# Kernel tuning notes

Measured on AMD Instinct MI355X. Metric: run time of the kernel, lower is better.

## Reference

```python
import jax, jax.numpy as jnp
import numpy as np

B, S, D, H = 4, 2048, 768, 12
DK = D // H


def setup_inputs() -> dict:
    key = jax.random.key(0)
    ks = jax.random.split(key, 12)
    s = 1.0 / np.sqrt(D)
    return {
        "query": jax.random.normal(ks[0], (B, S, D), jnp.float32),
        "key_": jax.random.normal(ks[1], (B, S, D), jnp.float32),
        "value": jax.random.normal(ks[2], (B, S, D), jnp.float32),
        "mask": jax.random.randint(ks[3], (B, S), 0, 2, jnp.int32),
        # nn.Linear weights are (out_features, in_features); y = x @ W.T + b
        "Wq": jax.random.normal(ks[4], (D, D), jnp.float32) * s,
        "bq": jnp.zeros((D,), jnp.float32),
        "Wk": jax.random.normal(ks[5], (D, D), jnp.float32) * s,
        "bk": jnp.zeros((D,), jnp.float32),
        "Wv": jax.random.normal(ks[6], (D, D), jnp.float32) * s,
        "bv": jnp.zeros((D,), jnp.float32),
        "Wo": jax.random.normal(ks[7], (D, D), jnp.float32) * s,
        "bo": jnp.zeros((D,), jnp.float32),
    }


def reference(query, key_, value, mask, Wq, bq, Wk, bk, Wv, bv, Wo, bo):
    b = query.shape[0]
    # QKV projections, split heads: (B, S, D) -> (B, H, S, DK)
    def proj(x, W, bia):
        y = x @ W.T + bia
        return y.reshape(b, -1, H, DK).transpose(0, 2, 1, 3)

    q = proj(query, Wq, bq)
    k = proj(key_, Wk, bk)
    v = proj(value, Wv, bv)

    # Scaled dot-product attention with full [B, H, S, S] score matrix
    scores = jnp.einsum("bhqd,bhkd->bhqk", q, k) / jnp.sqrt(jnp.float32(DK))
    # mask: (B, S) broadcast over heads and query positions; masked_fill(mask==0, -1e9)
    scores = jnp.where(mask[:, None, None, :] == 0, jnp.float32(-1e9), scores)
    attn = jax.nn.softmax(scores, axis=-1)
    x = jnp.einsum("bhqk,bhkd->bhqd", attn, v)  # (B, H, S, DK)

    # merge heads and output projection
    x = x.transpose(0, 2, 1, 3).reshape(b, -1, H * DK)
    return x @ Wo.T + bo
```

## Files before the change

### kernel.cpp

```cpp
#include <hip/hip_runtime.h>
#include <math.h>

#define B_  4
#define S_  2048
#define D_  768
#define H_  12
#define DK_ 64
#define M_  (B_ * S_)
#define NBH_ (B_ * H_)

typedef float f32x4 __attribute__((ext_vector_type(4)));
typedef float f32x16 __attribute__((ext_vector_type(16)));
typedef __bf16 bf16x8 __attribute__((ext_vector_type(8)));
typedef unsigned u32x4v __attribute__((ext_vector_type(4)));

static __device__ __forceinline__ unsigned short f2bf(float f) {
    unsigned u = __builtin_bit_cast(unsigned, f);
    u += 0x7fffu + ((u >> 16) & 1u);
    return (unsigned short)(u >> 16);
}

static __device__ __forceinline__ unsigned cvt_pk_bf16(float lo, float hi) {
    unsigned r;
    asm("v_cvt_pk_bf16_f32 %0, %1, %2" : "=v"(r) : "v"(lo), "v"(hi));
    return r;
}

static __device__ __forceinline__ void proj_body(
    const float* __restrict__ X, const float* __restrict__ W,
    const float* __restrict__ bias, void* __restrict__ outp, const int mode,
    const float oscale)
{
    __shared__ __align__(16) unsigned short As[128 * 32];
    __shared__ __align__(16) unsigned short Bs[128 * 32];

    const int t  = threadIdx.x;
    const int l  = t & 63;
    const int w  = t >> 6;
    const int lr = l & 15;
    const int lg = l >> 4;
    const int wm = w >> 1;
    const int wn = w & 1;
    const int m0 = blockIdx.x * 128;
    const int n0 = blockIdx.y * 128;

    f32x4 acc[4][4];
#pragma unroll
    for (int mi = 0; mi < 4; mi++)
#pragma unroll
        for (int ni = 0; ni < 4; ni++) acc[mi][ni] = (f32x4){0.f, 0.f, 0.f, 0.f};

    const int fsw = (lr >> 1) & 3;

    for (int k0 = 0; k0 < D_; k0 += 32) {
#pragma unroll
        for (int i = 0; i < 2; i++) {
            int v    = t + i * 256;
            int row  = v >> 2;
            int so   = v & 3;
            const float* xp = X + (size_t)(m0 + row) * D_ + k0 + so * 8;
            float4 x0 = *(const float4*)(xp);
            float4 x1 = *(const float4*)(xp + 4);
            ushort4 pa, pb;
            pa.x = f2bf(x0.x); pa.y = f2bf(x0.y); pa.z = f2bf(x0.z); pa.w = f2bf(x0.w);
            pb.x = f2bf(x1.x); pb.y = f2bf(x1.y); pb.z = f2bf(x1.z); pb.w = f2bf(x1.w);
            int off = row * 32 + ((so ^ ((row >> 1) & 3)) << 3);
            *(ushort4*)&As[off]     = pa;
            *(ushort4*)&As[off + 4] = pb;

            const float* wp = W + (size_t)(n0 + row) * D_ + k0 + so * 8;
            float4 w0 = *(const float4*)(wp);
            float4 w1 = *(const float4*)(wp + 4);
            pa.x = f2bf(w0.x); pa.y = f2bf(w0.y); pa.z = f2bf(w0.z); pa.w = f2bf(w0.w);
            pb.x = f2bf(w1.x); pb.y = f2bf(w1.y); pb.z = f2bf(w1.z); pb.w = f2bf(w1.w);
            *(ushort4*)&Bs[off]     = pa;
            *(ushort4*)&Bs[off + 4] = pb;
        }
        __syncthreads();

        bf16x8 af[4], bfr[4];
#pragma unroll
        for (int mi = 0; mi < 4; mi++) {
            int row = wm * 64 + mi * 16 + lr;
            af[mi] = *(const bf16x8*)&As[row * 32 + ((lg ^ fsw) << 3)];
        }
#pragma unroll
        for (int ni = 0; ni < 4; ni++) {
            int row = wn * 64 + ni * 16 + lr;
            bfr[ni] = *(const bf16x8*)&Bs[row * 32 + ((lg ^ fsw) << 3)];
        }
#pragma unroll
        for (int mi = 0; mi < 4; mi++)
#pragma unroll
            for (int ni = 0; ni < 4; ni++)
                acc[mi][ni] = __builtin_amdgcn_mfma_f32_16x16x32_bf16(
                    af[mi], bfr[ni], acc[mi][ni], 0, 0, 0);
        __syncthreads();
    }

    const int mrow0 = m0 + wm * 64;
    const int ncol0 = n0 + wn * 64;
    if (mode == 1) {
        float* out = (float*)outp;
#pragma unroll
        for (int mi = 0; mi < 4; mi++)
#pragma unroll
            for (int ni = 0; ni < 4; ni++) {
                int n = ncol0 + ni * 16 + lr;
                float bv = bias[n];
#pragma unroll
                for (int j = 0; j < 4; j++) {
                    int m = mrow0 + mi * 16 + 4 * lg + j;
                    out[(size_t)m * D_ + n] = acc[mi][ni][j] + bv;
                }
            }
    } else if (mode == 0) {
        unsigned short* out = (unsigned short*)outp;
#pragma unroll
        for (int mi = 0; mi < 4; mi++)
#pragma unroll
            for (int ni = 0; ni < 4; ni++) {
                int n = ncol0 + ni * 16 + lr;
                int h = n >> 6, dk = n & 63;
                float bv = bias[n];
#pragma unroll
                for (int j = 0; j < 4; j++) {
                    int m = mrow0 + mi * 16 + 4 * lg + j;
                    int b = m >> 11, s = m & (S_ - 1);
                    out[((size_t)(b * H_ + h) * S_ + s) * DK_ + dk] =
                        f2bf((acc[mi][ni][j] + bv) * oscale);
                }
            }
    } else {
        unsigned short* out = (unsigned short*)outp;
#pragma unroll
        for (int mi = 0; mi < 4; mi++)
#pragma unroll
            for (int ni = 0; ni < 4; ni++) {
                int n = ncol0 + ni * 16 + lr;
                int h = n >> 6, dk = n & 63;
                float bv = bias[n];
                int m = mrow0 + mi * 16 + 4 * lg;
                int b = m >> 11, s = m & (S_ - 1);
                ushort4 o;
                o.x = f2bf(acc[mi][ni][0] + bv);
                o.y = f2bf(acc[mi][ni][1] + bv);
                o.z = f2bf(acc[mi][ni][2] + bv);
                o.w = f2bf(acc[mi][ni][3] + bv);
                *(ushort4*)&out[((size_t)(b * H_ + h) * DK_ + dk) * S_ + s] = o;
            }
    }
}

__global__ __launch_bounds__(256) void proj_qkv(
    const float* __restrict__ Xq, const float* __restrict__ Xk,
    const float* __restrict__ Xv,
    const float* __restrict__ Wq, const float* __restrict__ bq,
    const float* __restrict__ Wk, const float* __restrict__ bk,
    const float* __restrict__ Wv, const float* __restrict__ bv,
    unsigned short* __restrict__ Qb, unsigned short* __restrict__ Kb,
    unsigned short* __restrict__ VT)
{
    const int z = blockIdx.z;
    const float* X    = (z == 0) ? Xq : (z == 1) ? Xk : Xv;
    const float* W    = (z == 0) ? Wq : (z == 1) ? Wk : Wv;
    const float* bias = (z == 0) ? bq : (z == 1) ? bk : bv;
    void* out         = (z == 0) ? (void*)Qb : (z == 1) ? (void*)Kb : (void*)VT;
    const int mode    = (z == 2) ? 2 : 0;
    const float osc   = (z == 0) ? 0.125f : 1.0f;
    proj_body(X, W, bias, out, mode, osc);
}

__global__ __launch_bounds__(256) void proj_mfma(
    const float* __restrict__ X, const float* __restrict__ W,
    const float* __restrict__ bias, void* __restrict__ outp, const int mode,
    const float oscale)
{
    proj_body(X, W, bias, outp, mode, oscale);
}

__global__ __launch_bounds__(256) void attn_mfma(
    const unsigned short* __restrict__ Qb, const unsigned short* __restrict__ Kb,
    const unsigned short* __restrict__ VTb, const int* __restrict__ mask,
    float* __restrict__ O)
{
    __shared__ __align__(16) unsigned short Ks[2][64 * 64];
    __shared__ __align__(16) unsigned short Vs[2][64 * 64];

    const int tid = threadIdx.x;
    const int w  = tid >> 6;
    const int l  = tid & 63;
    const int q  = l & 31;
    const int hl = l >> 5;

    const int bh = blockIdx.x % NBH_;
    const int qt = blockIdx.x / NBH_;
    const int b  = bh / H_;
    const int hh = bh - b * H_;
    const int q0 = qt * 128 + w * 32;

    const unsigned short* qp = Qb + ((size_t)bh * S_ + q0 + q) * DK_;
    bf16x8 qf[4];
#pragma unroll
    for (int c = 0; c < 4; c++)
        qf[c] = *(const bf16x8*)(qp + c * 16 + hl * 8);

    const unsigned qext_sel = (hl == 0) ? 0x00003F80u : 0u;
    const unsigned bias_sel = (hl == 0) ? 0x0000C480u : 0u;
    u32x4v qe; qe.x = qext_sel; qe.y = 0u; qe.z = 0u; qe.w = 0u;
    const bf16x8 qf_ext = __builtin_bit_cast(bf16x8, qe);
    u32x4v on; on.x = on.y = on.z = on.w = 0x3F803F80u;
    const bf16x8 vOnes = __builtin_bit_cast(bf16x8, on);

    f32x16 acc0, acc1, accl;
#pragma unroll
    for (int i = 0; i < 16; i++) { acc0[i] = 0.f; acc1[i] = 0.f; accl[i] = 0.f; }

    const unsigned short* kbase = Kb + (size_t)bh * S_ * DK_;
    const unsigned short* vbase = VTb + (size_t)bh * DK_ * S_;
    const int* mbase = mask + b * S_;

    const int row0 = tid >> 3,         slot0 = tid & 7;
    const int row1 = (tid + 256) >> 3, slot1 = (tid + 256) & 7;
    const int ld0 = row0 * 64 + ((slot0 * 8) ^ ((row0 & 7) << 3));
    const int ld1 = row1 * 64 + ((slot1 * 8) ^ ((row1 & 7) << 3));
    const unsigned short* kg0 = kbase + row0 * DK_ + slot0 * 8;
    const unsigned short* kg1 = kbase + row1 * DK_ + slot1 * 8;
    const unsigned short* vg0 = vbase + (size_t)row0 * S_ + slot0 * 8;
    const unsigned short* vg1 = vbase + (size_t)row1 * S_ + slot1 * 8;

    {
        int4 kr0 = *(const int4*)(kg0);
        int4 kr1 = *(const int4*)(kg1);
        int4 vr0 = *(const int4*)(vg0);
        int4 vr1 = *(const int4*)(vg1);
        *(int4*)&Ks[0][ld0] = kr0;
        *(int4*)&Ks[0][ld1] = kr1;
        *(int4*)&Vs[0][ld0] = vr0;
        *(int4*)&Vs[0][ld1] = vr1;
    }
    __syncthreads();

    const int fsw = (q & 7) << 3;

    for (int tt = 0; tt < 32; tt++) {
        const int j0  = tt * 64;
        const int cur = tt & 1;
        const bool more = (tt < 31);

        int4 kr0, kr1, vr0, vr1;
        if (more) {
            kr0 = *(const int4*)(kg0 + (size_t)(j0 + 64) * DK_);
            kr1 = *(const int4*)(kg1 + (size_t)(j0 + 64) * DK_);
            vr0 = *(const int4*)(vg0 + (j0 + 64));
            vr1 = *(const int4*)(vg1 + (j0 + 64));
        }

        int mv0 = mbase[j0 + q];
        int mv1 = mbase[j0 + 32 + q];
        u32x4v bw0; bw0.x = (mv0 == 0) ? bias_sel : 0u; bw0.y = 0u; bw0.z = 0u; bw0.w = 0u;
        u32x4v bw1; bw1.x = (mv1 == 0) ? bias_sel : 0u; bw1.y = 0u; bw1.z = 0u; bw1.w = 0u;
        bf16x8 kExt0 = __builtin_bit_cast(bf16x8, bw0);
        bf16x8 kExt1 = __builtin_bit_cast(bf16x8, bw1);

        bf16x8 kA[2][4];
#pragma unroll
        for (int kf = 0; kf < 2; kf++)
#pragma unroll
            for (int c = 0; c < 4; c++)
                kA[kf][c] = *(const bf16x8*)&Ks[cur][(32 * kf + q) * 64 +
                                ((c * 16 + hl * 8) ^ fsw)];

        f32x16 s0, s1;
#pragma unroll
        for (int i = 0; i < 16; i++) { s0[i] = 0.f; s1[i] = 0.f; }
        __builtin_amdgcn_s_setprio(1);
#pragma unroll
        for (int c = 0; c < 4; c++) {
            s0 = __builtin_amdgcn_mfma_f32_32x32x16_bf16(kA[0][c], qf[c], s0, 0, 0, 0);
            s1 = __builtin_amdgcn_mfma_f32_32x32x16_bf16(kA[1][c], qf[c], s1, 0, 0, 0);
        }
        s0 = __builtin_amdgcn_mfma_f32_32x32x16_bf16(kExt0, qf_ext, s0, 0, 0, 0);
        s1 = __builtin_amdgcn_mfma_f32_32x32x16_bf16(kExt1, qf_ext, s1, 0, 0, 0);
        __builtin_amdgcn_s_setprio(0);

        bf16x8 vA[2][4];
#pragma unroll
        for (int db = 0; db < 2; db++)
#pragma unroll
            for (int c = 0; c < 4; c++)
                vA[db][c] = *(const bf16x8*)&Vs[cur][(32 * db + q) * 64 +
                                ((c * 16 + hl * 8) ^ fsw)];

        float pv[2][16];
#pragma unroll
        for (int r = 0; r < 16; r++) pv[0][r] = __expf(s0[r]);
#pragma unroll
        for (int r = 0; r < 16; r++) pv[1][r] = __expf(s1[r]);

        bf16x8 pb[4];
#pragma unroll
        for (int cp = 0; cp < 4; cp++) {
            const int kfi = cp >> 1;
            const int e0  = 8 * (cp & 1);
            unsigned lo0 = cvt_pk_bf16(pv[kfi][e0 + 0], pv[kfi][e0 + 1]);
            unsigned hi0 = cvt_pk_bf16(pv[kfi][e0 + 2], pv[kfi][e0 + 3]);
            unsigned lo1 = cvt_pk_bf16(pv[kfi][e0 + 4], pv[kfi][e0 + 5]);
            unsigned hi1 = cvt_pk_bf16(pv[kfi][e0 + 6], pv[kfi][e0 + 7]);
            asm("v_permlane32_swap_b32 %0, %1" : "+v"(lo0), "+v"(lo1));
            asm("v_permlane32_swap_b32 %0, %1" : "+v"(hi0), "+v"(hi1));
            u32x4v pw;
            pw.x = lo0; pw.y = hi0; pw.z = lo1; pw.w = hi1;
            pb[cp] = __builtin_bit_cast(bf16x8, pw);
        }

        __builtin_amdgcn_s_setprio(1);
#pragma unroll
        for (int cp = 0; cp < 4; cp++) {
            acc0 = __builtin_amdgcn_mfma_f32_32x32x16_bf16(vA[0][cp], pb[cp], acc0, 0, 0, 0);
            acc1 = __builtin_amdgcn_mfma_f32_32x32x16_bf16(vA[1][cp], pb[cp], acc1, 0, 0, 0);
            accl = __builtin_amdgcn_mfma_f32_32x32x16_bf16(vOnes,    pb[cp], accl, 0, 0, 0);
        }
        __builtin_amdgcn_s_setprio(0);

        if (more) {
            *(int4*)&Ks[cur ^ 1][ld0] = kr0;
            *(int4*)&Ks[cur ^ 1][ld1] = kr1;
            *(int4*)&Vs[cur ^ 1][ld0] = vr0;
            *(int4*)&Vs[cur ^ 1][ld1] = vr1;
        }
        __syncthreads();
    }

    float inv = 1.f / accl[0];
    float* ob = O + ((size_t)b * S_ + q0 + q) * D_ + hh * DK_;
#pragma unroll
    for (int b2 = 0; b2 < 4; b2++) {
        float4 o;
        o.x = acc0[4 * b2 + 0] * inv;
        o.y = acc0[4 * b2 + 1] * inv;
        o.z = acc0[4 * b2 + 2] * inv;
        o.w = acc0[4 * b2 + 3] * inv;
        *(float4*)(ob + 8 * b2 + 4 * hl) = o;
    }
#pragma unroll
    for (int b2 = 0; b2 < 4; b2++) {
        float4 o;
        o.x = acc1[4 * b2 + 0] * inv;
        o.y = acc1[4 * b2 + 1] * inv;
        o.z = acc1[4 * b2 + 2] * inv;
        o.w = acc1[4 * b2 + 3] * inv;
        *(float4*)(ob + 32 + 8 * b2 + 4 * hl) = o;
    }
}

extern "C" void kernel_launch(void* const* d_in, const int* in_sizes, int n_in,
                              void* d_out, int out_size, void* d_ws, size_t ws_size,
                              hipStream_t stream) {
    (void)in_sizes; (void)n_in; (void)out_size; (void)ws_size;

    const float* query = (const float*)d_in[0];
    const float* key_  = (const float*)d_in[1];
    const float* value = (const float*)d_in[2];
    const int*   mask  = (const int*)d_in[3];
    const float* Wq = (const float*)d_in[4];  const float* bq = (const float*)d_in[5];
    const float* Wk = (const float*)d_in[6];  const float* bk = (const float*)d_in[7];
    const float* Wv = (const float*)d_in[8];  const float* bv = (const float*)d_in[9];
    const float* Wo = (const float*)d_in[10]; const float* bo = (const float*)d_in[11];
    float* out = (float*)d_out;

    unsigned short* Qb = (unsigned short*)d_ws;
    unsigned short* Kb = Qb + (size_t)M_ * D_;
    unsigned short* VT = Kb + (size_t)M_ * D_;
    float*          Xb = (float*)(VT + (size_t)M_ * D_);

    dim3 gqkv(M_ / 128, D_ / 128, 3);
    proj_qkv<<<gqkv, 256, 0, stream>>>(query, key_, value,
                                       Wq, bq, Wk, bk, Wv, bv, Qb, Kb, VT);

    attn_mfma<<<dim3((S_ / 128) * NBH_), 256, 0, stream>>>(Qb, Kb, VT, mask, Xb);

    dim3 gproj(M_ / 128, D_ / 128);
    proj_mfma<<<gproj, 256, 0, stream>>>(Xb, Wo, bo, (void*)out, 1, 1.0f);
}
```

Measured before the change: 204.6 us.

## Double-buffer projection GEMM LDS tiles and prefetch next K-slice into registers

```diff
diff --git a/kernel.cpp b/kernel.cpp
--- a/kernel.cpp
+++ b/kernel.cpp
@@ -31,8 +31,8 @@
     const float* __restrict__ bias, void* __restrict__ outp, const int mode,
     const float oscale)
 {
-    __shared__ __align__(16) unsigned short As[128 * 32];
-    __shared__ __align__(16) unsigned short Bs[128 * 32];
+    __shared__ __align__(16) unsigned short As[2][128 * 32];
+    __shared__ __align__(16) unsigned short Bs[2][128 * 32];
 
     const int t  = threadIdx.x;
     const int l  = t & 63;
@@ -44,6 +44,40 @@
     const int m0 = blockIdx.x * 128;
     const int n0 = blockIdx.y * 128;
 
+    const int v0r = t >> 2,         v0s = t & 3;
+    const int v1r = (t + 256) >> 2, v1s = (t + 256) & 3;
+    const int off0 = v0r * 32 + ((v0s ^ ((v0r >> 1) & 3)) << 3);
+    const int off1 = v1r * 32 + ((v1s ^ ((v1r >> 1) & 3)) << 3);
+    const float* xg0 = X + (size_t)(m0 + v0r) * D_ + v0s * 8;
+    const float* xg1 = X + (size_t)(m0 + v1r) * D_ + v1s * 8;
+    const float* wg0 = W + (size_t)(n0 + v0r) * D_ + v0s * 8;
+    const float* wg1 = W + (size_t)(n0 + v1r) * D_ + v1s * 8;
+
+    float4 pxa, pxb, pxc, pxd, pwa, pwb, pwc, pwd;
+
+#define PROJ_LOAD(K0) do { \
+        pxa = *(const float4*)(xg0 + (K0)); pxb = *(const float4*)(xg0 + (K0) + 4); \
+        pxc = *(const float4*)(xg1 + (K0)); pxd = *(const float4*)(xg1 + (K0) + 4); \
+        pwa = *(const float4*)(wg0 + (K0)); pwb = *(const float4*)(wg0 + (K0) + 4); \
+        pwc = *(const float4*)(wg1 + (K0)); pwd = *(const float4*)(wg1 + (K0) + 4); \
+    } while (0)
+
+#define PROJ_STORE(BUF) do { \
+        u32x4v xa_, xb_, wa_, wb_; \
+        xa_.x = cvt_pk_bf16(pxa.x, pxa.y); xa_.y = cvt_pk_bf16(pxa.z, pxa.w); \
+        xa_.z = cvt_pk_bf16(pxb.x, pxb.y); xa_.w = cvt_pk_bf16(pxb.z, pxb.w); \
+        xb_.x = cvt_pk_bf16(pxc.x, pxc.y); xb_.y = cvt_pk_bf16(pxc.z, pxc.w); \
+        xb_.z = cvt_pk_bf16(pxd.x, pxd.y); xb_.w = cvt_pk_bf16(pxd.z, pxd.w); \
+        wa_.x = cvt_pk_bf16(pwa.x, pwa.y); wa_.y = cvt_pk_bf16(pwa.z, pwa.w); \
+        wa_.z = cvt_pk_bf16(pwb.x, pwb.y); wa_.w = cvt_pk_bf16(pwb.z, pwb.w); \
+        wb_.x = cvt_pk_bf16(pwc.x, pwc.y); wb_.y = cvt_pk_bf16(pwc.z, pwc.w); \
+        wb_.z = cvt_pk_bf16(pwd.x, pwd.y); wb_.w = cvt_pk_bf16(pwd.z, pwd.w); \
+        *(u32x4v*)&As[BUF][off0] = xa_; \
+        *(u32x4v*)&As[BUF][off1] = xb_; \
+        *(u32x4v*)&Bs[BUF][off0] = wa_; \
+        *(u32x4v*)&Bs[BUF][off1] = wb_; \
+    } while (0)
+
     f32x4 acc[4][4];
 #pragma unroll
     for (int mi = 0; mi < 4; mi++)
@@ -52,42 +86,26 @@
 
     const int fsw = (lr >> 1) & 3;
 
-    for (int k0 = 0; k0 < D_; k0 += 32) {
-#pragma unroll
-        for (int i = 0; i < 2; i++) {
-            int v    = t + i * 256;
-            int row  = v >> 2;
-            int so   = v & 3;
-            const float* xp = X + (size_t)(m0 + row) * D_ + k0 + so * 8;
-            float4 x0 = *(const float4*)(xp);
-            float4 x1 = *(const float4*)(xp + 4);
-            ushort4 pa, pb;
-            pa.x = f2bf(x0.x); pa.y = f2bf(x0.y); pa.z = f2bf(x0.z); pa.w = f2bf(x0.w);
-            pb.x = f2bf(x1.x); pb.y = f2bf(x1.y); pb.z = f2bf(x1.z); pb.w = f2bf(x1.w);
-            int off = row * 32 + ((so ^ ((row >> 1) & 3)) << 3);
-            *(ushort4*)&As[off]     = pa;
-            *(ushort4*)&As[off + 4] = pb;
-
-            const float* wp = W + (size_t)(n0 + row) * D_ + k0 + so * 8;
-            float4 w0 = *(const float4*)(wp);
-            float4 w1 = *(const float4*)(wp + 4);
-            pa.x = f2bf(w0.x); pa.y = f2bf(w0.y); pa.z = f2bf(w0.z); pa.w = f2bf(w0.w);
-            pb.x = f2bf(w1.x); pb.y = f2bf(w1.y); pb.z = f2bf(w1.z); pb.w = f2bf(w1.w);
-            *(ushort4*)&Bs[off]     = pa;
-            *(ushort4*)&Bs[off + 4] = pb;
-        }
-        __syncthreads();
+    PROJ_LOAD(0);
+    PROJ_STORE(0);
+    __syncthreads();
+
+    for (int kt = 0; kt < 24; kt++) {
+        const int cur = kt & 1;
+        const bool more = (kt < 23);
+
+        if (more) PROJ_LOAD((kt + 1) * 32);
 
         bf16x8 af[4], bfr[4];
 #pragma unroll
         for (int mi = 0; mi < 4; mi++) {
             int row = wm * 64 + mi * 16 + lr;
-            af[mi] = *(const bf16x8*)&As[row * 32 + ((lg ^ fsw) << 3)];
+            af[mi] = *(const bf16x8*)&As[cur][row * 32 + ((lg ^ fsw) << 3)];
         }
 #pragma unroll
         for (int ni = 0; ni < 4; ni++) {
             int row = wn * 64 + ni * 16 + lr;
-            bfr[ni] = *(const bf16x8*)&Bs[row * 32 + ((lg ^ fsw) << 3)];
+            bfr[ni] = *(const bf16x8*)&Bs[cur][row * 32 + ((lg ^ fsw) << 3)];
         }
 #pragma unroll
         for (int mi = 0; mi < 4; mi++)
@@ -95,8 +113,13 @@
             for (int ni = 0; ni < 4; ni++)
                 acc[mi][ni] = __builtin_amdgcn_mfma_f32_16x16x32_bf16(
                     af[mi], bfr[ni], acc[mi][ni], 0, 0, 0);
+
+        if (more) PROJ_STORE(cur ^ 1);
         __syncthreads();
     }
+
+#undef PROJ_LOAD
+#undef PROJ_STORE
 
     const int mrow0 = m0 + wm * 64;
     const int ncol0 = n0 + wn * 64;
@@ -142,12 +165,10 @@
                 float bv = bias[n];
                 int m = mrow0 + mi * 16 + 4 * lg;
                 int b = m >> 11, s = m & (S_ - 1);
-                ushort4 o;
-                o.x = f2bf(acc[mi][ni][0] + bv);
-                o.y = f2bf(acc[mi][ni][1] + bv);
-                o.z = f2bf(acc[mi][ni][2] + bv);
-                o.w = f2bf(acc[mi][ni][3] + bv);
-                *(ushort4*)&out[((size_t)(b * H_ + h) * DK_ + dk) * S_ + s] = o;
+                uint2 o;
+                o.x = cvt_pk_bf16(acc[mi][ni][0] + bv, acc[mi][ni][1] + bv);
+                o.y = cvt_pk_bf16(acc[mi][ni][2] + bv, acc[mi][ni][3] + bv);
+                *(uint2*)&out[((size_t)(b * H_ + h) * DK_ + dk) * S_ + s] = o;
             }
     }
 }
```

Measured after the change: 184.9 us. 9.6% less time.
